# Optimization experiments

Measured on AMD Instinct MI355X. Metric: run time of the kernel, lower is better.

Reference implementation:

```python
import jax, jax.numpy as jnp
import numpy as np

WINDOW_SIZE = 11
SIGMA = 1.5
C1 = 0.01 ** 2
C2 = 0.03 ** 2


def _gaussian_window(window_size: int, channel: int) -> jnp.ndarray:
    # 1D gaussian, normalized
    g = jnp.arange(window_size, dtype=jnp.float32) - window_size // 2
    g = jnp.exp(-(g ** 2) / (2.0 * SIGMA ** 2))
    g = g / g.sum()
    w2d = jnp.outer(g, g)  # [K, K]
    # depthwise conv kernel: [C, 1, K, K] in OIHW with feature_group_count=C
    return jnp.broadcast_to(w2d[None, None], (channel, 1, window_size, window_size))


def _depthwise_conv(x: jnp.ndarray, window: jnp.ndarray, channel: int) -> jnp.ndarray:
    pad = WINDOW_SIZE // 2
    return jax.lax.conv_general_dilated(
        x, window,
        window_strides=(1, 1),
        padding=((pad, pad), (pad, pad)),
        dimension_numbers=('NCHW', 'OIHW', 'NCHW'),
        feature_group_count=channel,
    )


def setup_inputs() -> dict:
    key = jax.random.key(0)
    k1, k2 = jax.random.split(key)
    shape = (16, 3, 512, 512)
    img1 = jax.random.uniform(k1, shape, dtype=jnp.float32)
    img2 = jax.random.uniform(k2, shape, dtype=jnp.float32)
    return {"img1": img1, "img2": img2}


def reference(img1, img2):
    channel = img1.shape[1]
    window = _gaussian_window(WINDOW_SIZE, channel).astype(img1.dtype)

    mu1 = _depthwise_conv(img1, window, channel)
    mu2 = _depthwise_conv(img2, window, channel)

    mu1_sq = mu1 * mu1
    mu2_sq = mu2 * mu2
    mu1_mu2 = mu1 * mu2

    sigma1_sq = _depthwise_conv(img1 * img1, window, channel) - mu1_sq
    sigma2_sq = _depthwise_conv(img2 * img2, window, channel) - mu2_sq
    sigma12 = _depthwise_conv(img1 * img2, window, channel) - mu1_mu2

    ssim_map = ((2.0 * mu1_mu2 + C1) * (2.0 * sigma12 + C2)) / (
        (mu1_sq + mu2_sq + C1) * (sigma1_sq + sigma2_sq + C2))

    return 1.0 - ssim_map.mean()
```

## Files before the change

kernel.cpp:

```cpp
#include <hip/hip_runtime.h>

#define IMG_W 512
#define IMG_H 512
#define PLANE_PX (IMG_W * IMG_H)
#define N_ELEMS (48 * PLANE_PX)
#define NTHREADS 256
#define TILEW 54
#define NCT 10
#define NBLK (48 * 16 * NCT)
#define RSTR 66

#define C1f 1.0e-4f
#define C2f 9.0e-4f

typedef _Float16 h2 __attribute__((ext_vector_type(2)));
typedef __fp16 fp16v2 __attribute__((ext_vector_type(2)));

__device__ __forceinline__ h2 h2fma(_Float16 w, h2 v, h2 acc) {
    h2 wv = {w, w};
    return __builtin_elementwise_fma(wv, v, acc);
}
__device__ __forceinline__ unsigned int h2bits(h2 v) {
    union { h2 h; unsigned int u; } c; c.h = v; return c.u;
}
__device__ __forceinline__ h2 bits2h(unsigned int u) {
    union { h2 h; unsigned int u; } c; c.u = u; return c.h;
}
__device__ __forceinline__ h2 pkrtz(float x, float y) {
    union { fp16v2 f; h2 h; } c;
    c.f = __builtin_amdgcn_cvt_pkrtz(x, y);
    return c.h;
}

__global__ void __launch_bounds__(NTHREADS, 8) ssim_main(
    const float* __restrict__ img1, const float* __restrict__ img2,
    float* __restrict__ partials)
{
    __shared__ uint2 R[32 * RSTR];
    __shared__ float wpart[4];

    constexpr _Float16 Gh[11] = {
        (_Float16)0.00102838f, (_Float16)0.00759876f, (_Float16)0.03600077f,
        (_Float16)0.10936070f, (_Float16)0.21300553f, (_Float16)0.26601173f,
        (_Float16)0.21300553f, (_Float16)0.10936070f, (_Float16)0.03600077f,
        (_Float16)0.00759876f, (_Float16)0.00102838f
    };

    const int tid = threadIdx.x;

    const int xcd = blockIdx.x & 7;
    const int idx = blockIdx.x >> 3;
    const int plane = xcd * 6 + idx / 160;
    const int t = idx % 160;
    const int band = t / 10;
    const int ct = t - band * 10;
    const int tx0 = ct * TILEW;
    const int ty0 = band * 32;
    const float* pa = img1 + (size_t)plane * PLANE_PX;
    const float* pb = img2 + (size_t)plane * PLANE_PX;

    const int c = tid & 63;
    const int g = tid >> 6;
    const int gx = tx0 - 5 + c;
    const int cgx = min(max(gx, 0), IMG_W - 1);
    const _Float16 ml = ((unsigned)gx < (unsigned)IMG_W) ? (_Float16)1.f
                                                         : (_Float16)0.f;
    const h2 mlv = {ml, ml};
    const int ry0 = ty0 + g * 8 - 5;

    float av[18], bv[18];
    const bool intY = (ry0 >= 0) && (ry0 + 18 <= IMG_H);
    if (intY) {
        const float* qa = pa + (size_t)ry0 * IMG_W + cgx;
        const float* qb = pb + (size_t)ry0 * IMG_W + cgx;
#pragma unroll
        for (int j = 0; j < 18; ++j) {
            av[j] = qa[j * IMG_W];
            bv[j] = qb[j * IMG_W];
        }
    } else {
#pragma unroll
        for (int j = 0; j < 18; ++j) {
            int ry = ry0 + j;
            int ryc = min(max(ry, 0), IMG_H - 1);
            float rm = ((unsigned)ry < (unsigned)IMG_H) ? 1.f : 0.f;
            av[j] = pa[(size_t)ryc * IMG_W + cgx] * rm;
            bv[j] = pb[(size_t)ryc * IMG_W + cgx] * rm;
        }
    }

    h2 asd[8], asq[8];
#pragma unroll
    for (int k = 0; k < 8; ++k) { asd[k] = (h2)(_Float16)0; asq[k] = (h2)(_Float16)0; }
#pragma unroll
    for (int j = 0; j < 18; ++j) {
        h2 sd = pkrtz(av[j] + bv[j], av[j] - bv[j]);
        h2 sq = sd * sd;
#pragma unroll
        for (int k = 0; k < 8; ++k) {
            int tt = j - k;
            if (tt >= 0 && tt < 11) {
                asd[k] = h2fma(Gh[tt], sd, asd[k]);
                asq[k] = h2fma(Gh[tt], sq, asq[k]);
            }
        }
    }
#pragma unroll
    for (int k = 0; k < 8; ++k) {
        h2 wsd = asd[k] * mlv;
        h2 wsq = asq[k] * mlv;
        R[(g * 8 + k) * RSTR + c] = make_uint2(h2bits(wsd), h2bits(wsq));
    }
    __syncthreads();

    const int y = tid >> 3;
    const int cg = tid & 7;
    const int c0 = cg * 7;
    const uint2* row = R + y * RSTR;

    h2 osd[7], osq[7];
#pragma unroll
    for (int o = 0; o < 7; ++o) { osd[o] = (h2)(_Float16)0; osq[o] = (h2)(_Float16)0; }

#pragma unroll
    for (int j = 0; j < 17; ++j) {
        uint2 p = row[min(c0 + j, 65)];
        h2 vsd = bits2h(p.x);
        h2 vsq = bits2h(p.y);
#pragma unroll
        for (int o = 0; o < 7; ++o) {
            int tt = j - o;
            if (tt >= 0 && tt < 11) {
                osd[o] = h2fma(Gh[tt], vsd, osd[o]);
                osq[o] = h2fma(Gh[tt], vsq, osq[o]);
            }
        }
    }

    float local = 0.f;
#pragma unroll
    for (int o = 0; o < 7; ++o) {
        float cs  = (float)osd[o].x, cd  = (float)osd[o].y;
        float css = (float)osq[o].x, cdd = (float)osq[o].y;
        float cs2 = cs * cs, cd2 = cd * cd;
        float mu12 = 0.25f * (cs2 - cd2);
        float musq = 0.50f * (cs2 + cd2);
        float e12  = 0.25f * (css - cdd);
        float esum = 0.50f * (css + cdd);
        float num = (2.f * mu12 + C1f) * (2.f * (e12 - mu12) + C2f);
        float den = (musq + C1f) * ((esum - musq) + C2f);
        float sv = num * __builtin_amdgcn_rcpf(den);
        bool valid = (c0 + o < TILEW) && (tx0 + c0 + o < IMG_W);
        local += valid ? sv : 0.f;
    }

#pragma unroll
    for (int off = 32; off > 0; off >>= 1) local += __shfl_down(local, off, 64);
    if ((tid & 63) == 0) wpart[tid >> 6] = local;
    __syncthreads();
    if (tid == 0)
        partials[blockIdx.x] = wpart[0] + wpart[1] + wpart[2] + wpart[3];
}

__global__ void ssim_final(const float* __restrict__ partials,
                           float* __restrict__ out)
{
    __shared__ float wp[4];
    const int tid = threadIdx.x;
    const float4* p4 = (const float4*)partials;
    float s = 0.f;
    for (int i = tid; i < NBLK / 4; i += NTHREADS) {
        float4 v = p4[i];
        s += (v.x + v.y) + (v.z + v.w);
    }
#pragma unroll
    for (int off = 32; off > 0; off >>= 1) s += __shfl_down(s, off, 64);
    if ((tid & 63) == 0) wp[tid >> 6] = s;
    __syncthreads();
    if (tid == 0)
        out[0] = 1.0f - (wp[0] + wp[1] + wp[2] + wp[3]) * (1.0f / (float)N_ELEMS);
}

extern "C" void kernel_launch(void* const* d_in, const int* in_sizes, int n_in,
                              void* d_out, int out_size, void* d_ws, size_t ws_size,
                              hipStream_t stream) {
    const float* img1 = (const float*)d_in[0];
    const float* img2 = (const float*)d_in[1];
    float* out = (float*)d_out;
    float* partials = (float*)d_ws;

    ssim_main<<<NBLK, NTHREADS, 0, stream>>>(img1, img2, partials);
    ssim_final<<<1, NTHREADS, 0, stream>>>(partials, out);
}
```

Baseline: 133.4 us.

## Run horizontal Gaussian pass as MFMA Toeplitz matmul with taller tiles

Replaces the per-thread scalar horizontal 11-tap convolution with 16x16x32 f16 MFMA instructions. A banded Toeplitz weight matrix is built in registers with lane shuffles and multiplied against row data read from an XOR-swizzled LDS tile. Tiles grow to 64 rows by 48 output columns, so fewer vertical halo rows are loaded again, and the column mask is applied only on edge tiles. The SSIM formula is refolded to drop the scale factors. The larger register arrays lower the occupancy target from 8 to 5 blocks, and the MFMA computes some padded work.

```diff
diff --git a/kernel.cpp b/kernel.cpp
--- a/kernel.cpp
+++ b/kernel.cpp
@@ -5,15 +5,17 @@
 #define PLANE_PX (IMG_W * IMG_H)
 #define N_ELEMS (48 * PLANE_PX)
 #define NTHREADS 256
-#define TILEW 54
-#define NCT 10
-#define NBLK (48 * 16 * NCT)
-#define RSTR 66
-
-#define C1f 1.0e-4f
-#define C2f 9.0e-4f
+#define TILEW 48
+#define NCT 11
+#define NBANDS 8
+#define NBLK (48 * NBANDS * NCT)
+
+#define C1x2 2.0e-4f
+#define C2x2 1.8e-3f
 
 typedef _Float16 h2 __attribute__((ext_vector_type(2)));
+typedef _Float16 h8 __attribute__((ext_vector_type(8)));
+typedef float f32x4 __attribute__((ext_vector_type(4)));
 typedef __fp16 fp16v2 __attribute__((ext_vector_type(2)));
 
 __device__ __forceinline__ h2 h2fma(_Float16 w, h2 v, h2 acc) {
@@ -22,9 +24,6 @@
 }
 __device__ __forceinline__ unsigned int h2bits(h2 v) {
     union { h2 h; unsigned int u; } c; c.h = v; return c.u;
-}
-__device__ __forceinline__ h2 bits2h(unsigned int u) {
-    union { h2 h; unsigned int u; } c; c.u = u; return c.h;
 }
 __device__ __forceinline__ h2 pkrtz(float x, float y) {
     union { fp16v2 f; h2 h; } c;
@@ -32,12 +31,11 @@
     return c.h;
 }
 
-__global__ void __launch_bounds__(NTHREADS, 8) ssim_main(
+__global__ void __launch_bounds__(NTHREADS, 5) ssim_main(
     const float* __restrict__ img1, const float* __restrict__ img2,
     float* __restrict__ partials)
 {
-    __shared__ uint2 R[32 * RSTR];
-    __shared__ float wpart[4];
+    __shared__ __align__(16) uint2 R[64 * 64];
 
     constexpr _Float16 Gh[11] = {
         (_Float16)0.00102838f, (_Float16)0.00759876f, (_Float16)0.03600077f,
@@ -50,12 +48,12 @@
 
     const int xcd = blockIdx.x & 7;
     const int idx = blockIdx.x >> 3;
-    const int plane = xcd * 6 + idx / 160;
-    const int t = idx % 160;
-    const int band = t / 10;
-    const int ct = t - band * 10;
+    const int plane = xcd * 6 + idx / 88;
+    const int t = idx % 88;
+    const int band = t / 11;
+    const int ct = t - band * 11;
     const int tx0 = ct * TILEW;
-    const int ty0 = band * 32;
+    const int ty0 = band * 64;
     const float* pa = img1 + (size_t)plane * PLANE_PX;
     const float* pb = img2 + (size_t)plane * PLANE_PX;
 
@@ -63,24 +61,21 @@
     const int g = tid >> 6;
     const int gx = tx0 - 5 + c;
     const int cgx = min(max(gx, 0), IMG_W - 1);
-    const _Float16 ml = ((unsigned)gx < (unsigned)IMG_W) ? (_Float16)1.f
-                                                         : (_Float16)0.f;
-    const h2 mlv = {ml, ml};
-    const int ry0 = ty0 + g * 8 - 5;
-
-    float av[18], bv[18];
-    const bool intY = (ry0 >= 0) && (ry0 + 18 <= IMG_H);
+    const int ry0 = ty0 + g * 16 - 5;
+
+    float av[26], bv[26];
+    const bool intY = (ry0 >= 0) && (ry0 + 26 <= IMG_H);
     if (intY) {
         const float* qa = pa + (size_t)ry0 * IMG_W + cgx;
         const float* qb = pb + (size_t)ry0 * IMG_W + cgx;
 #pragma unroll
-        for (int j = 0; j < 18; ++j) {
+        for (int j = 0; j < 26; ++j) {
             av[j] = qa[j * IMG_W];
             bv[j] = qb[j * IMG_W];
         }
     } else {
 #pragma unroll
-        for (int j = 0; j < 18; ++j) {
+        for (int j = 0; j < 26; ++j) {
             int ry = ry0 + j;
             int ryc = min(max(ry, 0), IMG_H - 1);
             float rm = ((unsigned)ry < (unsigned)IMG_H) ? 1.f : 0.f;
@@ -89,15 +84,15 @@
         }
     }
 
-    h2 asd[8], asq[8];
-#pragma unroll
-    for (int k = 0; k < 8; ++k) { asd[k] = (h2)(_Float16)0; asq[k] = (h2)(_Float16)0; }
-#pragma unroll
-    for (int j = 0; j < 18; ++j) {
+    h2 asd[16], asq[16];
+#pragma unroll
+    for (int k = 0; k < 16; ++k) { asd[k] = (h2)(_Float16)0; asq[k] = (h2)(_Float16)0; }
+#pragma unroll
+    for (int j = 0; j < 26; ++j) {
         h2 sd = pkrtz(av[j] + bv[j], av[j] - bv[j]);
         h2 sq = sd * sd;
 #pragma unroll
-        for (int k = 0; k < 8; ++k) {
+        for (int k = 0; k < 16; ++k) {
             int tt = j - k;
             if (tt >= 0 && tt < 11) {
                 asd[k] = h2fma(Gh[tt], sd, asd[k]);
@@ -105,61 +100,102 @@
             }
         }
     }
-#pragma unroll
-    for (int k = 0; k < 8; ++k) {
-        h2 wsd = asd[k] * mlv;
-        h2 wsq = asq[k] * mlv;
-        R[(g * 8 + k) * RSTR + c] = make_uint2(h2bits(wsd), h2bits(wsq));
-    }
-    __syncthreads();
-
-    const int y = tid >> 3;
-    const int cg = tid & 7;
-    const int c0 = cg * 7;
-    const uint2* row = R + y * RSTR;
-
-    h2 osd[7], osq[7];
-#pragma unroll
-    for (int o = 0; o < 7; ++o) { osd[o] = (h2)(_Float16)0; osq[o] = (h2)(_Float16)0; }
-
-#pragma unroll
-    for (int j = 0; j < 17; ++j) {
-        uint2 p = row[min(c0 + j, 65)];
-        h2 vsd = bits2h(p.x);
-        h2 vsq = bits2h(p.y);
-#pragma unroll
-        for (int o = 0; o < 7; ++o) {
-            int tt = j - o;
-            if (tt >= 0 && tt < 11) {
-                osd[o] = h2fma(Gh[tt], vsd, osd[o]);
-                osq[o] = h2fma(Gh[tt], vsq, osq[o]);
+
+    if (ct == 0 || ct == NCT - 1) {
+        const _Float16 ml = ((unsigned)gx < (unsigned)IMG_W) ? (_Float16)1.f
+                                                             : (_Float16)0.f;
+        const h2 mlv = {ml, ml};
+#pragma unroll
+        for (int k = 0; k < 16; ++k) { asd[k] = asd[k] * mlv; asq[k] = asq[k] * mlv; }
+    }
+#pragma unroll
+    for (int kk = 0; kk < 16; ++kk) {
+        const int row = g * 16 + kk;
+        const int sc = c ^ ((kk & 7) << 1);
+        R[row * 64 + sc] = make_uint2(h2bits(asd[kk]), h2bits(asq[kk]));
+    }
+    __syncthreads();
+
+    const int lane = tid & 63;
+    const int nrow = lane & 15;
+    const int khi = lane >> 4;
+    const int rs = tid >> 6;
+    const int row_lds = rs * 16 + nrow;
+    const int swz = (nrow & 7) << 1;
+    const uint2* Rrow = R + row_lds * 64;
+
+    int sidx = min(lane, 10 - lane);
+    unsigned gvb = 0u;
+    gvb = (sidx == 0) ? 0x1436u : gvb;
+    gvb = (sidx == 1) ? 0x1FC8u : gvb;
+    gvb = (sidx == 2) ? 0x289Cu : gvb;
+    gvb = (sidx == 3) ? 0x2F00u : gvb;
+    gvb = (sidx == 4) ? 0x32D1u : gvb;
+    gvb = (sidx == 5) ? 0x3442u : gvb;
+    union { h8 h; unsigned u[4]; } af;
+#pragma unroll
+    for (int w = 0; w < 4; ++w) {
+        int t0 = khi * 8 + 2 * w - nrow;
+        unsigned lo = (unsigned)__shfl((int)gvb, t0 & 63, 64);
+        unsigned hi = (unsigned)__shfl((int)gvb, (t0 + 1) & 63, 64);
+        af.u[w] = (lo & 0xFFFFu) | (hi << 16);
+    }
+
+    float local = 0.f;
+#pragma unroll
+    for (int mg = 0; mg < 3; ++mg) {
+        if (tx0 + mg * 16 < IMG_W) {
+            const int cb = mg * 16 + khi * 8;
+            const uint4 q0 = *(const uint4*)&Rrow[(cb + 0) ^ swz];
+            const uint4 q1 = *(const uint4*)&Rrow[(cb + 2) ^ swz];
+            const uint4 q2 = *(const uint4*)&Rrow[(cb + 4) ^ swz];
+            const uint4 q3 = *(const uint4*)&Rrow[(cb + 6) ^ swz];
+
+            union { h8 h; unsigned u[4]; } fs, fd, fss, fdd;
+            fs.u[0]  = (q0.x & 0xFFFFu) | (q0.z << 16);
+            fs.u[1]  = (q1.x & 0xFFFFu) | (q1.z << 16);
+            fs.u[2]  = (q2.x & 0xFFFFu) | (q2.z << 16);
+            fs.u[3]  = (q3.x & 0xFFFFu) | (q3.z << 16);
+            fd.u[0]  = (q0.x >> 16) | (q0.z & 0xFFFF0000u);
+            fd.u[1]  = (q1.x >> 16) | (q1.z & 0xFFFF0000u);
+            fd.u[2]  = (q2.x >> 16) | (q2.z & 0xFFFF0000u);
+            fd.u[3]  = (q3.x >> 16) | (q3.z & 0xFFFF0000u);
+            fss.u[0] = (q0.y & 0xFFFFu) | (q0.w << 16);
+            fss.u[1] = (q1.y & 0xFFFFu) | (q1.w << 16);
+            fss.u[2] = (q2.y & 0xFFFFu) | (q2.w << 16);
+            fss.u[3] = (q3.y & 0xFFFFu) | (q3.w << 16);
+            fdd.u[0] = (q0.y >> 16) | (q0.w & 0xFFFF0000u);
+            fdd.u[1] = (q1.y >> 16) | (q1.w & 0xFFFF0000u);
+            fdd.u[2] = (q2.y >> 16) | (q2.w & 0xFFFF0000u);
+            fdd.u[3] = (q3.y >> 16) | (q3.w & 0xFFFF0000u);
+
+            const f32x4 z = {0.f, 0.f, 0.f, 0.f};
+            f32x4 aS  = __builtin_amdgcn_mfma_f32_16x16x32_f16(af.h, fs.h,  z, 0, 0, 0);
+            f32x4 aD  = __builtin_amdgcn_mfma_f32_16x16x32_f16(af.h, fd.h,  z, 0, 0, 0);
+            f32x4 aSS = __builtin_amdgcn_mfma_f32_16x16x32_f16(af.h, fss.h, z, 0, 0, 0);
+            f32x4 aDD = __builtin_amdgcn_mfma_f32_16x16x32_f16(af.h, fdd.h, z, 0, 0, 0);
+
+#pragma unroll
+            for (int i = 0; i < 4; ++i) {
+                float cs = aS[i], cd = aD[i], css = aSS[i], cdd = aDD[i];
+                float P = cs * cs, Q = cd * cd;
+                float U = P - Q;
+                float V = P + Q;
+                float num = (U + C1x2) * ((css - cdd) - U + C2x2);
+                float den = (V + C1x2) * ((css + cdd) - V + C2x2);
+                local += num * __builtin_amdgcn_rcpf(den);
             }
         }
     }
 
-    float local = 0.f;
-#pragma unroll
-    for (int o = 0; o < 7; ++o) {
-        float cs  = (float)osd[o].x, cd  = (float)osd[o].y;
-        float css = (float)osq[o].x, cdd = (float)osq[o].y;
-        float cs2 = cs * cs, cd2 = cd * cd;
-        float mu12 = 0.25f * (cs2 - cd2);
-        float musq = 0.50f * (cs2 + cd2);
-        float e12  = 0.25f * (css - cdd);
-        float esum = 0.50f * (css + cdd);
-        float num = (2.f * mu12 + C1f) * (2.f * (e12 - mu12) + C2f);
-        float den = (musq + C1f) * ((esum - musq) + C2f);
-        float sv = num * __builtin_amdgcn_rcpf(den);
-        bool valid = (c0 + o < TILEW) && (tx0 + c0 + o < IMG_W);
-        local += valid ? sv : 0.f;
-    }
-
 #pragma unroll
     for (int off = 32; off > 0; off >>= 1) local += __shfl_down(local, off, 64);
-    if ((tid & 63) == 0) wpart[tid >> 6] = local;
+    __syncthreads();
+    float* wp = (float*)R;
+    if (lane == 0) wp[rs] = local;
     __syncthreads();
     if (tid == 0)
-        partials[blockIdx.x] = wpart[0] + wpart[1] + wpart[2] + wpart[3];
+        partials[blockIdx.x] = wp[0] + wp[1] + wp[2] + wp[3];
 }
 
 __global__ void ssim_final(const float* __restrict__ partials,
```

Result: faster. 127.8 us (-4.2%).
